# Kernel optimization log

Hardware: AMD Instinct MI355X
Metric: run time of the kernel (lower is better)

The kernel has to match this reference:

```python
import jax, jax.numpy as jnp
import numpy as np

B, S, D = 4, 2048, 1024
H = 16
HD = D // H  # 64

def setup_inputs() -> dict:
    key = jax.random.key(0)
    ks = jax.random.split(key, 7)
    s = 0.02
    return {
        "x": jax.random.normal(ks[0], (B, S, D), dtype=jnp.float32),
        "Wq": jax.random.normal(ks[1], (D, D), dtype=jnp.float32) * s,
        "bq": jax.random.normal(ks[2], (D,), dtype=jnp.float32) * s,
        "Wk": jax.random.normal(ks[3], (D, D), dtype=jnp.float32) * s,
        "bk": jax.random.normal(ks[4], (D,), dtype=jnp.float32) * s,
        "Wv": jax.random.normal(ks[5], (D, D), dtype=jnp.float32) * s,
        "bv": jax.random.normal(ks[6], (D,), dtype=jnp.float32) * s,
    }

def reference(x, Wq, bq, Wk, bk, Wv, bv):
    bs, seq, _ = x.shape
    q = (x @ Wq.T + bq).reshape(bs, seq, H, HD).transpose(0, 2, 1, 3)  # [b,h,s,d]
    k = (x @ Wk.T + bk).reshape(bs, seq, H, HD).transpose(0, 2, 1, 3)
    v = (x @ Wv.T + bv).reshape(bs, seq, H, HD).transpose(0, 2, 1, 3)
    scores = jnp.einsum('bhqd,bhkd->bhqk', q, k) / jnp.sqrt(jnp.float32(HD))
    probs = jax.nn.softmax(scores, axis=-1)  # dropout p=0 -> identity
    att = jnp.einsum('bhqk,bhkd->bhqd', probs, v)
    return att.transpose(0, 2, 1, 3).reshape(bs, seq, H * HD)
```

## Files before the change

kernel.cpp:

```cpp
#include <hip/hip_runtime.h>

typedef __bf16 bf16x8 __attribute__((ext_vector_type(8)));
typedef float f32x4 __attribute__((ext_vector_type(4)));

#define BATCH 4
#define SEQ   2048
#define DIM   1024
#define NH    16
#define HD    64
#define ECF   0.18033688f

__device__ __forceinline__ unsigned short f2bf(float f) {
  union { float f; unsigned u; } v; v.f = f;
  unsigned u = v.u;
  u += 0x7FFF + ((u >> 16) & 1);
  return (unsigned short)(u >> 16);
}

__device__ __forceinline__ void g2lds16(const unsigned short* g, unsigned short* l) {
  __builtin_amdgcn_global_load_lds(
      (const __attribute__((address_space(1))) unsigned int*)g,
      (__attribute__((address_space(3))) unsigned int*)l, 16, 0, 0);
}

__global__ __launch_bounds__(256) void cast_all_kernel(
    const float* __restrict__ x,  const float* __restrict__ Wq,
    const float* __restrict__ Wk, const float* __restrict__ Wv,
    unsigned short* __restrict__ xb,  unsigned short* __restrict__ wqb,
    unsigned short* __restrict__ wkb, unsigned short* __restrict__ wvb) {
  const int XG = (BATCH * SEQ * DIM) / 8;
  const int WG = (DIM * DIM) / 8;
  int i = blockIdx.x * 256 + threadIdx.x;
  const float* in; unsigned short* out; float sc = 1.0f; int off;
  if (i < XG)               { in = x;  out = xb;  off = i; }
  else if (i < XG + WG)     { in = Wq; out = wqb; off = i - XG; sc = ECF; }
  else if (i < XG + 2 * WG) { in = Wk; out = wkb; off = i - XG - WG; }
  else                      { in = Wv; out = wvb; off = i - XG - 2 * WG; }
  const float4* p = (const float4*)in + (size_t)off * 2;
  float4 a = p[0], b = p[1];
  unsigned short r[8];
  r[0] = f2bf(a.x * sc); r[1] = f2bf(a.y * sc); r[2] = f2bf(a.z * sc); r[3] = f2bf(a.w * sc);
  r[4] = f2bf(b.x * sc); r[5] = f2bf(b.y * sc); r[6] = f2bf(b.z * sc); r[7] = f2bf(b.w * sc);
  *(uint4*)&out[(size_t)off * 8] = *(uint4*)r;
}

__global__ __launch_bounds__(512, 1) void gemm_qkv(
    const unsigned short* __restrict__ A,
    const unsigned short* __restrict__ Wqp, const unsigned short* __restrict__ Wkp,
    const unsigned short* __restrict__ Wvp,
    const float* __restrict__ bqp, const float* __restrict__ bkp,
    const float* __restrict__ bvp,
    unsigned short* __restrict__ oq, unsigned short* __restrict__ ok,
    unsigned short* __restrict__ ov) {
  __shared__ __align__(16) unsigned short sm[3 * 24576];

  const int z = blockIdx.z;
  const unsigned short* W = (z == 0) ? Wqp : (z == 1) ? Wkp : Wvp;
  const float* bias        = (z == 0) ? bqp : (z == 1) ? bkp : bvp;
  unsigned short* outp     = (z == 0) ? oq  : (z == 1) ? ok  : ov;
  const float bsc          = (z == 0) ? ECF : 1.0f;
  const int mode = (z == 2) ? 1 : 0;

  const int tid  = threadIdx.x;
  const int w    = tid >> 6;
  const int lane = tid & 63;
  const int lm   = lane & 15;
  const int qd   = lane >> 4;
  const int m0 = blockIdx.x * 256;
  const int n0 = blockIdx.y * 128;
  const int wm = (w & 3) * 64;
  const int wn = (w >> 2) * 64;

  const f32x4 zero = {0.f, 0.f, 0.f, 0.f};
  f32x4 acc[4][4];
#pragma unroll
  for (int i = 0; i < 4; ++i)
#pragma unroll
    for (int j = 0; j < 4; ++j) acc[i][j] = zero;

  const int r0 = tid >> 3;
  const int sp = ((tid & 7) ^ (r0 & 7)) * 8;

#define SA(buf, t4, i) g2lds16(&A[(size_t)(m0 + r0 + 64*(i)) * DIM + (t4)*64 + sp], \
                               &sm[(buf)*24576 + (r0 + 64*(i))*64 + (tid & 7)*8])
#define SB(buf, t4, i) g2lds16(&W[(size_t)(n0 + r0 + 64*(i)) * DIM + (t4)*64 + sp], \
                               &sm[(buf)*24576 + 16384 + (r0 + 64*(i))*64 + (tid & 7)*8])
#define BARR() asm volatile("s_barrier" ::: "memory")

  const int rk = lm & 7;

  SA(0, 0, 0); SA(0, 0, 1); SA(0, 0, 2); SA(0, 0, 3); SB(0, 0, 0); SB(0, 0, 1);
  SA(1, 1, 0); SA(1, 1, 1); SA(1, 1, 2); SA(1, 1, 3); SB(1, 1, 0); SB(1, 1, 1);
  asm volatile("s_waitcnt vmcnt(6)" ::: "memory");
  BARR();

  for (int t = 0; t < DIM / 64; ++t) {
    const int cur = t % 3;
    const int nb  = (t + 2) % 3;
    const bool st = (t + 2) < DIM / 64;
    const unsigned short* Ab = &sm[cur * 24576];
    const unsigned short* Bb = &sm[cur * 24576 + 16384];

    {
      bf16x8 af[4], bfr[4];
#pragma unroll
      for (int i = 0; i < 4; ++i)
        af[i]  = *(const bf16x8*)&Ab[(wm + i * 16 + lm) * 64 + ((qd ^ rk) * 8)];
#pragma unroll
      for (int j = 0; j < 4; ++j)
        bfr[j] = *(const bf16x8*)&Bb[(wn + j * 16 + lm) * 64 + ((qd ^ rk) * 8)];
      if (st) { SA(nb, t + 2, 0); SA(nb, t + 2, 1); SA(nb, t + 2, 2); }
      BARR();
      __builtin_amdgcn_s_setprio(1);
#pragma unroll
      for (int i = 0; i < 4; ++i)
#pragma unroll
        for (int j = 0; j < 4; ++j)
          acc[i][j] = __builtin_amdgcn_mfma_f32_16x16x32_bf16(af[i], bfr[j], acc[i][j], 0, 0, 0);
      __builtin_amdgcn_s_setprio(0);
      BARR();
    }

    {
      bf16x8 af[4], bfr[4];
#pragma unroll
      for (int i = 0; i < 4; ++i)
        af[i]  = *(const bf16x8*)&Ab[(wm + i * 16 + lm) * 64 + (((4 + qd) ^ rk) * 8)];
#pragma unroll
      for (int j = 0; j < 4; ++j)
        bfr[j] = *(const bf16x8*)&Bb[(wn + j * 16 + lm) * 64 + (((4 + qd) ^ rk) * 8)];
      if (st) { SA(nb, t + 2, 3); SB(nb, t + 2, 0); SB(nb, t + 2, 1); }
      BARR();
      __builtin_amdgcn_s_setprio(1);
#pragma unroll
      for (int i = 0; i < 4; ++i)
#pragma unroll
        for (int j = 0; j < 4; ++j)
          acc[i][j] = __builtin_amdgcn_mfma_f32_16x16x32_bf16(af[i], bfr[j], acc[i][j], 0, 0, 0);
      __builtin_amdgcn_s_setprio(0);
      if (st) asm volatile("s_waitcnt vmcnt(6)" ::: "memory");
      else    asm volatile("s_waitcnt vmcnt(0)" ::: "memory");
      BARR();
    }
  }
#undef SA
#undef SB
#undef BARR

#pragma unroll
  for (int j = 0; j < 4; ++j) {
    int col = n0 + wn + j * 16 + lm;
    float bb = bias[col] * bsc;
    int h = col >> 6, hd = col & 63;
#pragma unroll
    for (int i = 0; i < 4; ++i) {
      int rowb = m0 + wm + i * 16 + qd * 4;
      int b = rowb >> 11, s = rowb & 2047;
      if (mode == 0) {
#pragma unroll
        for (int r = 0; r < 4; ++r) {
          float v = acc[i][j][r] + bb;
          outp[((size_t)(b * NH + h) * SEQ + (s + r)) * HD + hd] = f2bf(v);
        }
      } else {
        unsigned short pk[4];
#pragma unroll
        for (int r = 0; r < 4; ++r) pk[r] = f2bf(acc[i][j][r] + bb);
        size_t idx = ((size_t)(b * NH + h) * HD + hd) * SEQ + s;
        *(uint2*)&outp[idx] = *(uint2*)pk;
      }
    }
  }
}

__global__ __launch_bounds__(128, 2) void flash_kernel(
    const unsigned short* __restrict__ Qw, const unsigned short* __restrict__ Kw,
    const unsigned short* __restrict__ Vw, float* __restrict__ out) {
  __shared__ unsigned short Ks2[2 * 64 * 32];
  __shared__ unsigned short Vs2[2 * 64 * 32];
  __shared__ unsigned short Ps[128 * 64];
  __shared__ float Ls[128];

  const int tid  = threadIdx.x;
  const int w    = tid >> 6;
  const int lane = tid & 63;
  const int lm   = lane & 15;
  const int qd   = lane >> 4;
  const int bh   = blockIdx.y;
  const int q0   = blockIdx.x * 128;

  const unsigned short* Qbase = Qw + (size_t)bh * (SEQ * HD);
  const unsigned short* Kbase = Kw + (size_t)bh * (SEQ * HD);
  const unsigned short* Vbase = Vw + (size_t)bh * (HD * SEQ);

  bf16x8 qf[4][2];
#pragma unroll
  for (int g = 0; g < 4; ++g)
#pragma unroll
    for (int h = 0; h < 2; ++h)
      qf[g][h] = *(const bf16x8*)&Qbase[(size_t)(q0 + w * 64 + g * 16 + lm) * HD + h * 32 + qd * 8];

  const f32x4 zero = {0.f, 0.f, 0.f, 0.f};
  f32x4 o[4][4];
#pragma unroll
  for (int g = 0; g < 4; ++g)
#pragma unroll
    for (int jn = 0; jn < 4; ++jn) o[g][jn] = zero;
  float psg[4] = {0.f, 0.f, 0.f, 0.f};

  const int c0 = tid, c1 = tid + 128;
  const int r0 = c0 >> 2, p0s = ((c0 & 3) ^ ((c0 >> 3) & 3)) * 8;
  const int r1 = c1 >> 2, p1s = ((c1 & 3) ^ ((c1 >> 3) & 3)) * 8;

  const int cs  = (qd ^ ((lm >> 1) & 3)) * 8;
  const int pk_key = lm & 7;

  for (int kt = 0; kt < SEQ / 64; ++kt) {
    const int k0 = kt * 64;
    __syncthreads();
    g2lds16(&Kbase[(size_t)(k0 + r0) * HD + p0s],      &Ks2[(size_t)c0 * 8]);
    g2lds16(&Kbase[(size_t)(k0 + r1) * HD + p1s],      &Ks2[(size_t)c1 * 8]);
    g2lds16(&Kbase[(size_t)(k0 + r0) * HD + 32 + p0s], &Ks2[2048 + (size_t)c0 * 8]);
    g2lds16(&Kbase[(size_t)(k0 + r1) * HD + 32 + p1s], &Ks2[2048 + (size_t)c1 * 8]);
    g2lds16(&Vbase[(size_t)r0 * SEQ + k0 + p0s],       &Vs2[(size_t)c0 * 8]);
    g2lds16(&Vbase[(size_t)r1 * SEQ + k0 + p1s],       &Vs2[(size_t)c1 * 8]);
    g2lds16(&Vbase[(size_t)r0 * SEQ + k0 + 32 + p0s],  &Vs2[2048 + (size_t)c0 * 8]);
    g2lds16(&Vbase[(size_t)r1 * SEQ + k0 + 32 + p1s],  &Vs2[2048 + (size_t)c1 * 8]);
    __syncthreads();

#pragma unroll
    for (int jk = 0; jk < 4; ++jk) {
      bf16x8 kf0 = *(const bf16x8*)&Ks2[(jk * 16 + lm) * 32 + cs];
      bf16x8 kf1 = *(const bf16x8*)&Ks2[2048 + (jk * 16 + lm) * 32 + cs];
      f32x4 st[4];
#pragma unroll
      for (int g = 0; g < 4; ++g) {
        st[g] = __builtin_amdgcn_mfma_f32_16x16x32_bf16(kf0, qf[g][0], zero, 0, 0, 0);
        st[g] = __builtin_amdgcn_mfma_f32_16x16x32_bf16(kf1, qf[g][1], st[g], 0, 0, 0);
      }
#pragma unroll
      for (int g = 0; g < 4; ++g) {
        float p0 = __builtin_amdgcn_exp2f(st[g][0]);
        float p1 = __builtin_amdgcn_exp2f(st[g][1]);
        float p2 = __builtin_amdgcn_exp2f(st[g][2]);
        float p3 = __builtin_amdgcn_exp2f(st[g][3]);
        psg[g] += (p0 + p1) + (p2 + p3);
        uint2 pk;
        pk.x = __builtin_amdgcn_perm(__float_as_uint(p1), __float_as_uint(p0), 0x07060302);
        pk.y = __builtin_amdgcn_perm(__float_as_uint(p3), __float_as_uint(p2), 0x07060302);
        int sw = (2 * jk + (qd >> 1)) ^ pk_key;
        *(uint2*)&Ps[(w * 64 + g * 16 + lm) * 64 + sw * 8 + (qd & 1) * 4] = pk;
      }
    }

    asm volatile("s_waitcnt lgkmcnt(0)" ::: "memory");

#pragma unroll
    for (int h2 = 0; h2 < 2; ++h2) {
      bf16x8 pf[4];
#pragma unroll
      for (int g = 0; g < 4; ++g) {
        int sw = (h2 * 4 + qd) ^ pk_key;
        pf[g] = *(const bf16x8*)&Ps[(w * 64 + g * 16 + lm) * 64 + sw * 8];
      }
#pragma unroll
      for (int jn = 0; jn < 4; ++jn) {
        bf16x8 vf = *(const bf16x8*)&Vs2[h2 * 2048 + (jn * 16 + lm) * 32 + cs];
#pragma unroll
        for (int g = 0; g < 4; ++g)
          o[g][jn] = __builtin_amdgcn_mfma_f32_16x16x32_bf16(pf[g], vf, o[g][jn], 0, 0, 0);
      }
    }
  }

#pragma unroll
  for (int g = 0; g < 4; ++g) {
    float l = psg[g];
    l += __shfl_xor(l, 16); l += __shfl_xor(l, 32);
    if (qd == 0) Ls[w * 64 + g * 16 + lm] = l;
  }
  asm volatile("s_waitcnt lgkmcnt(0)" ::: "memory");

  const int b = bh >> 4, hh = bh & 15;
#pragma unroll
  for (int g = 0; g < 4; ++g)
#pragma unroll
    for (int r = 0; r < 4; ++r) {
      float inv = 1.0f / Ls[w * 64 + g * 16 + qd * 4 + r];
      int qrow = q0 + w * 64 + g * 16 + qd * 4 + r;
#pragma unroll
      for (int jn = 0; jn < 4; ++jn)
        out[(size_t)(b * SEQ + qrow) * DIM + hh * HD + jn * 16 + lm] = o[g][jn][r] * inv;
    }
}

extern "C" void kernel_launch(void* const* d_in, const int* in_sizes, int n_in,
                              void* d_out, int out_size, void* d_ws, size_t ws_size,
                              hipStream_t stream) {
  const float* x  = (const float*)d_in[0];
  const float* Wq = (const float*)d_in[1];
  const float* bq = (const float*)d_in[2];
  const float* Wk = (const float*)d_in[3];
  const float* bk = (const float*)d_in[4];
  const float* Wv = (const float*)d_in[5];
  const float* bv = (const float*)d_in[6];
  float* out = (float*)d_out;

  unsigned short* ws = (unsigned short*)d_ws;
  const size_t XE = (size_t)BATCH * SEQ * DIM;
  const size_t WE = (size_t)DIM * DIM;
  unsigned short* xb  = ws;
  unsigned short* wqb = xb + XE;
  unsigned short* wkb = wqb + WE;
  unsigned short* wvb = wkb + WE;
  unsigned short* qb  = wvb + WE;
  unsigned short* kb  = qb + XE;
  unsigned short* vb  = kb + XE;

  const int total_groups = (int)(XE / 8 + 3 * (WE / 8));
  cast_all_kernel<<<total_groups / 256, 256, 0, stream>>>(
      x, Wq, Wk, Wv, xb, wqb, wkb, wvb);

  dim3 gg(32, 8, 3);
  gemm_qkv<<<gg, 512, 0, stream>>>(xb, wqb, wkb, wvb, bq, bk, bv, qb, kb, vb);

  dim3 fg(SEQ / 128, BATCH * NH);
  flash_kernel<<<fg, 128, 0, stream>>>(qb, kb, vb, out);
}
```

Baseline: 242.6 us.

## Enlarge QKV GEMM tile to 256x256 with double-buffered LDS pipeline

```diff
diff --git a/kernel.cpp b/kernel.cpp
--- a/kernel.cpp
+++ b/kernel.cpp
@@ -52,7 +52,7 @@
     const float* __restrict__ bvp,
     unsigned short* __restrict__ oq, unsigned short* __restrict__ ok,
     unsigned short* __restrict__ ov) {
-  __shared__ __align__(16) unsigned short sm[3 * 24576];
+  __shared__ __align__(16) unsigned short sm[2 * 32768];
 
   const int z = blockIdx.z;
   const unsigned short* W = (z == 0) ? Wqp : (z == 1) ? Wkp : Wvp;
@@ -67,50 +67,52 @@
   const int lm   = lane & 15;
   const int qd   = lane >> 4;
   const int m0 = blockIdx.x * 256;
-  const int n0 = blockIdx.y * 128;
-  const int wm = (w & 3) * 64;
-  const int wn = (w >> 2) * 64;
-
-  const f32x4 zero = {0.f, 0.f, 0.f, 0.f};
-  f32x4 acc[4][4];
-#pragma unroll
-  for (int i = 0; i < 4; ++i)
-#pragma unroll
-    for (int j = 0; j < 4; ++j) acc[i][j] = zero;
+  const int n0 = blockIdx.y * 256;
+  const int wm = (w & 1) * 128;
+  const int wn = (w >> 1) * 64;
+
+  f32x4 acc[8][4];
+#pragma unroll
+  for (int i = 0; i < 8; ++i)
+#pragma unroll
+    for (int j = 0; j < 4; ++j) acc[i][j] = {0.f, 0.f, 0.f, 0.f};
 
   const int r0 = tid >> 3;
   const int sp = ((tid & 7) ^ (r0 & 7)) * 8;
 
 #define SA(buf, t4, i) g2lds16(&A[(size_t)(m0 + r0 + 64*(i)) * DIM + (t4)*64 + sp], \
-                               &sm[(buf)*24576 + (r0 + 64*(i))*64 + (tid & 7)*8])
+                               &sm[(buf)*32768 + (r0 + 64*(i))*64 + (tid & 7)*8])
 #define SB(buf, t4, i) g2lds16(&W[(size_t)(n0 + r0 + 64*(i)) * DIM + (t4)*64 + sp], \
-                               &sm[(buf)*24576 + 16384 + (r0 + 64*(i))*64 + (tid & 7)*8])
+                               &sm[(buf)*32768 + 16384 + (r0 + 64*(i))*64 + (tid & 7)*8])
 #define BARR() asm volatile("s_barrier" ::: "memory")
 
   const int rk = lm & 7;
 
-  SA(0, 0, 0); SA(0, 0, 1); SA(0, 0, 2); SA(0, 0, 3); SB(0, 0, 0); SB(0, 0, 1);
-  SA(1, 1, 0); SA(1, 1, 1); SA(1, 1, 2); SA(1, 1, 3); SB(1, 1, 0); SB(1, 1, 1);
-  asm volatile("s_waitcnt vmcnt(6)" ::: "memory");
+  SA(0, 0, 0); SA(0, 0, 1); SA(0, 0, 2); SA(0, 0, 3);
+  SB(0, 0, 0); SB(0, 0, 1); SB(0, 0, 2); SB(0, 0, 3);
+  asm volatile("s_waitcnt vmcnt(0)" ::: "memory");
   BARR();
 
+  int cur = 0;
   for (int t = 0; t < DIM / 64; ++t) {
-    const int cur = t % 3;
-    const int nb  = (t + 2) % 3;
-    const bool st = (t + 2) < DIM / 64;
-    const unsigned short* Ab = &sm[cur * 24576];
-    const unsigned short* Bb = &sm[cur * 24576 + 16384];
+    const unsigned short* Ab = &sm[cur * 32768];
+    const unsigned short* Bb = &sm[cur * 32768 + 16384];
+
+    if (t + 1 < DIM / 64) {
+      SA(cur ^ 1, t + 1, 0); SA(cur ^ 1, t + 1, 1);
+      SA(cur ^ 1, t + 1, 2); SA(cur ^ 1, t + 1, 3);
+      SB(cur ^ 1, t + 1, 0); SB(cur ^ 1, t + 1, 1);
+      SB(cur ^ 1, t + 1, 2); SB(cur ^ 1, t + 1, 3);
+    }
 
     {
-      bf16x8 af[4], bfr[4];
-#pragma unroll
-      for (int i = 0; i < 4; ++i)
-        af[i]  = *(const bf16x8*)&Ab[(wm + i * 16 + lm) * 64 + ((qd ^ rk) * 8)];
+      bf16x8 bfr[4], af[4];
 #pragma unroll
       for (int j = 0; j < 4; ++j)
         bfr[j] = *(const bf16x8*)&Bb[(wn + j * 16 + lm) * 64 + ((qd ^ rk) * 8)];
-      if (st) { SA(nb, t + 2, 0); SA(nb, t + 2, 1); SA(nb, t + 2, 2); }
-      BARR();
+#pragma unroll
+      for (int i = 0; i < 4; ++i)
+        af[i] = *(const bf16x8*)&Ab[(wm + i * 16 + lm) * 64 + ((qd ^ rk) * 8)];
       __builtin_amdgcn_s_setprio(1);
 #pragma unroll
       for (int i = 0; i < 4; ++i)
@@ -118,19 +120,25 @@
         for (int j = 0; j < 4; ++j)
           acc[i][j] = __builtin_amdgcn_mfma_f32_16x16x32_bf16(af[i], bfr[j], acc[i][j], 0, 0, 0);
       __builtin_amdgcn_s_setprio(0);
-      BARR();
-    }
-
+#pragma unroll
+      for (int i = 0; i < 4; ++i)
+        af[i] = *(const bf16x8*)&Ab[(wm + (4 + i) * 16 + lm) * 64 + ((qd ^ rk) * 8)];
+      __builtin_amdgcn_s_setprio(1);
+#pragma unroll
+      for (int i = 0; i < 4; ++i)
+#pragma unroll
+        for (int j = 0; j < 4; ++j)
+          acc[4 + i][j] = __builtin_amdgcn_mfma_f32_16x16x32_bf16(af[i], bfr[j], acc[4 + i][j], 0, 0, 0);
+      __builtin_amdgcn_s_setprio(0);
+    }
     {
-      bf16x8 af[4], bfr[4];
-#pragma unroll
-      for (int i = 0; i < 4; ++i)
-        af[i]  = *(const bf16x8*)&Ab[(wm + i * 16 + lm) * 64 + (((4 + qd) ^ rk) * 8)];
+      bf16x8 bfr[4], af[4];
 #pragma unroll
       for (int j = 0; j < 4; ++j)
         bfr[j] = *(const bf16x8*)&Bb[(wn + j * 16 + lm) * 64 + (((4 + qd) ^ rk) * 8)];
-      if (st) { SA(nb, t + 2, 3); SB(nb, t + 2, 0); SB(nb, t + 2, 1); }
-      BARR();
+#pragma unroll
+      for (int i = 0; i < 4; ++i)
+        af[i] = *(const bf16x8*)&Ab[(wm + i * 16 + lm) * 64 + (((4 + qd) ^ rk) * 8)];
       __builtin_amdgcn_s_setprio(1);
 #pragma unroll
       for (int i = 0; i < 4; ++i)
@@ -138,10 +146,21 @@
         for (int j = 0; j < 4; ++j)
           acc[i][j] = __builtin_amdgcn_mfma_f32_16x16x32_bf16(af[i], bfr[j], acc[i][j], 0, 0, 0);
       __builtin_amdgcn_s_setprio(0);
-      if (st) asm volatile("s_waitcnt vmcnt(6)" ::: "memory");
-      else    asm volatile("s_waitcnt vmcnt(0)" ::: "memory");
-      BARR();
-    }
+#pragma unroll
+      for (int i = 0; i < 4; ++i)
+        af[i] = *(const bf16x8*)&Ab[(wm + (4 + i) * 16 + lm) * 64 + (((4 + qd) ^ rk) * 8)];
+      __builtin_amdgcn_s_setprio(1);
+#pragma unroll
+      for (int i = 0; i < 4; ++i)
+#pragma unroll
+        for (int j = 0; j < 4; ++j)
+          acc[4 + i][j] = __builtin_amdgcn_mfma_f32_16x16x32_bf16(af[i], bfr[j], acc[4 + i][j], 0, 0, 0);
+      __builtin_amdgcn_s_setprio(0);
+    }
+
+    asm volatile("s_waitcnt vmcnt(0)" ::: "memory");
+    BARR();
+    cur ^= 1;
   }
 #undef SA
 #undef SB
@@ -153,7 +172,7 @@
     float bb = bias[col] * bsc;
     int h = col >> 6, hd = col & 63;
 #pragma unroll
-    for (int i = 0; i < 4; ++i) {
+    for (int i = 0; i < 8; ++i) {
       int rowb = m0 + wm + i * 16 + qd * 4;
       int b = rowb >> 11, s = rowb & 2047;
       if (mode == 0) {
@@ -321,7 +340,7 @@
   cast_all_kernel<<<total_groups / 256, 256, 0, stream>>>(
       x, Wq, Wk, Wv, xb, wqb, wkb, wvb);
 
-  dim3 gg(32, 8, 3);
+  dim3 gg(32, 4, 3);
   gemm_qkv<<<gg, 512, 0, stream>>>(xb, wqb, wkb, wvb, bq, bk, bv, qb, kb, vb);
 
   dim3 fg(SEQ / 128, BATCH * NH);
```

Result: slower. 250.7 us (+3.3%).
